# Optimization experiments

Measured on AMD Instinct MI355X. Metric: run time of the kernel, lower is better.

The kernel has to match this reference:

```python
import jax, jax.numpy as jnp
import numpy as np

B = 131072
UNITS = 256
INPUT_DIM = 256


def setup_inputs() -> dict:
    key = jax.random.key(0)
    ks = jax.random.split(key, 8)
    x = jax.random.normal(ks[0], (B, INPUT_DIM), dtype=jnp.float32)
    h_prev = jax.random.normal(ks[1], (B, UNITS), dtype=jnp.float32)
    c_prev = jax.random.normal(ks[2], (B, UNITS), dtype=jnp.float32)
    # glorot-like scale for W: fan_in = INPUT_DIM + UNITS, fan_out = 4*UNITS
    scale = jnp.sqrt(2.0 / (INPUT_DIM + UNITS + 4 * UNITS)).astype(jnp.float32)
    W = jax.random.normal(ks[3], (INPUT_DIM + UNITS, 4 * UNITS), dtype=jnp.float32) * scale
    # bias: zeros except forget gate initialized to 1.0
    b = jnp.concatenate([
        jnp.zeros(UNITS, jnp.float32),
        jnp.ones(UNITS, jnp.float32),
        jnp.zeros(UNITS, jnp.float32),
        jnp.zeros(UNITS, jnp.float32),
    ])
    peephole_i = jax.random.normal(ks[4], (UNITS,), dtype=jnp.float32) * 0.05
    peephole_f = jax.random.normal(ks[5], (UNITS,), dtype=jnp.float32) * 0.05
    peephole_o = jax.random.normal(ks[6], (UNITS,), dtype=jnp.float32) * 0.05
    return {
        "x": x, "h_prev": h_prev, "c_prev": c_prev,
        "W": W, "b": b,
        "peephole_i": peephole_i, "peephole_f": peephole_f, "peephole_o": peephole_o,
    }


def reference(x, h_prev, c_prev, W, b, peephole_i, peephole_f, peephole_o):
    combined = jnp.concatenate([x, h_prev], axis=-1)          # [B, INPUT_DIM+UNITS]
    z = combined @ W + b                                      # [B, 4*UNITS]
    i, f, c_hat, o = jnp.split(z, 4, axis=1)                  # each [B, UNITS]
    i = jax.nn.sigmoid(i + peephole_i * c_prev)
    f = jax.nn.sigmoid(f + peephole_f * c_prev)
    o = jax.nn.sigmoid(o + peephole_o * c_prev)
    c_hat = jnp.tanh(c_hat)
    c = f * c_prev + i * c_hat
    h = o * jnp.tanh(c)
    return (h, h, c)  # matches (output, [h, c]) of the Keras cell
```

## Files before the change

kernel.cpp:

```cpp
#include <hip/hip_runtime.h>
#include <cstdint>

#define NROWS   131072
#define NUNITS  256
#define KTOT    512
#define BM      128
#define THREADS 512

typedef float f32x4  __attribute__((ext_vector_type(4)));
typedef short bf16x8 __attribute__((ext_vector_type(8)));

__device__ __forceinline__ short f2bf(float x) {
    unsigned u = __float_as_uint(x);
    u += 0x7FFFu + ((u >> 16) & 1u);
    return (short)(u >> 16);
}

__global__ void convert_kernel(const float* __restrict__ x, const float* __restrict__ h,
                               const float* __restrict__ W,
                               short* __restrict__ Aws, short* __restrict__ Wws) {
    int b = blockIdx.x;
    if (b < 32768) {
        int i = b * 256 + threadIdx.x;
        int row = i >> 6;
        int c   = (i & 63) * 4;
        float4 xv = *(const float4*)(x + (size_t)row * 256 + c);
        float4 hv = *(const float4*)(h + (size_t)row * 256 + c);
        short xs[4] = {f2bf(xv.x), f2bf(xv.y), f2bf(xv.z), f2bf(xv.w)};
        short hs[4] = {f2bf(hv.x), f2bf(hv.y), f2bf(hv.z), f2bf(hv.w)};
        *(uint2*)(Aws + (size_t)row * 512 + c)       = *(uint2*)xs;
        *(uint2*)(Aws + (size_t)row * 512 + 256 + c) = *(uint2*)hs;
    } else {
        int i = (b - 32768) * 256 + threadIdx.x;
        int k = i >> 10;
        int c = i & 1023;
        Wws[((size_t)(k >> 5) << 15) + ((size_t)c << 5) + (k & 31)] = f2bf(W[i]);
    }
}

__global__ void __launch_bounds__(THREADS, 4)
lstm_main_kernel(const float* __restrict__ c_prev, const float* __restrict__ bias,
                 const float* __restrict__ pi, const float* __restrict__ pf,
                 const float* __restrict__ po, const short* __restrict__ Aws,
                 const short* __restrict__ Wws, float* __restrict__ out) {
    __shared__ short lds[3][12288];

    const int bid = blockIdx.x;
    const int swz = (bid & 7) * 512 + (bid >> 3);
    const int ut  = swz & 3;
    const int rt  = swz >> 2;
    const int row0 = rt * BM;

    const int t    = threadIdx.x;
    const int lane = t & 63;
    const int w    = t >> 6;
    const int lr   = lane & 15;
    const int hi   = lane >> 4;
    const int rh   = w >> 2;
    const int q    = w & 3;

    const int arow = t >> 2, ags = t & 3;
    const short* srcA = Aws + (size_t)(row0 + arow) * 512 + ((ags ^ (arow & 3)) * 8);
    const int G1 = t + 512;
    const int g0 = t >> 8,  u0 = (t >> 2) & 63,  s0 = t & 3;
    const int g1 = G1 >> 8, u1 = (G1 >> 2) & 63, s1 = G1 & 3;
    const short* srcB0 = Wws + (size_t)(g0 * 256 + ut * 64 + u0) * 32 + ((s0 ^ (u0 & 3)) * 8);
    const short* srcB1 = Wws + (size_t)(g1 * 256 + ut * 64 + u1) * 32 + ((s1 ^ (u1 & 3)) * 8);

    const int sw8  = (hi ^ (lr & 3)) * 8;
    const int aoff = (rh * 64 + lr) * 32 + sw8;
    const int boff = 4096 + (q * 16 + lr) * 32 + sw8;

    f32x4 acc[4][4];
    #pragma unroll
    for (int m = 0; m < 4; ++m)
        #pragma unroll
        for (int g = 0; g < 4; ++g)
            acc[m][g] = (f32x4){0.f, 0.f, 0.f, 0.f};

    auto issueDMA = [&](int ks, int buf) {
        short* dst = &lds[buf][0];
        __builtin_amdgcn_global_load_lds(
            (const __attribute__((address_space(1))) uint32_t*)(const void*)(srcA + ks * 32),
            (__attribute__((address_space(3))) uint32_t*)(void*)(dst + w * 512), 16, 0, 0);
        __builtin_amdgcn_global_load_lds(
            (const __attribute__((address_space(1))) uint32_t*)(const void*)(srcB0 + (size_t)ks * 32768),
            (__attribute__((address_space(3))) uint32_t*)(void*)(dst + 4096 + w * 512), 16, 0, 0);
        __builtin_amdgcn_global_load_lds(
            (const __attribute__((address_space(1))) uint32_t*)(const void*)(srcB1 + (size_t)ks * 32768),
            (__attribute__((address_space(3))) uint32_t*)(void*)(dst + 8192 + w * 512), 16, 0, 0);
    };

    auto compute = [&](int buf) {
        const short* L = &lds[buf][0];
        bf16x8 af[4], bfr[4];
        #pragma unroll
        for (int m = 0; m < 4; ++m)
            af[m] = *(const bf16x8*)&L[aoff + m * 512];
        #pragma unroll
        for (int g = 0; g < 4; ++g)
            bfr[g] = *(const bf16x8*)&L[boff + g * 2048];
        #pragma unroll
        for (int g = 0; g < 4; ++g)
            #pragma unroll
            for (int m = 0; m < 4; ++m)
                acc[m][g] = __builtin_amdgcn_mfma_f32_16x16x32_bf16(af[m], bfr[g], acc[m][g], 0, 0, 0);
    };

    issueDMA(0, 0);
    issueDMA(1, 1);

    int cur = 0;
    #pragma unroll 1
    for (int p = 0; p < 16; ++p) {
        if (p < 15) { asm volatile("s_waitcnt vmcnt(3)" ::: "memory"); }
        else        { asm volatile("s_waitcnt vmcnt(0)" ::: "memory"); }
        __builtin_amdgcn_s_barrier();
        if (p < 14) {
            int nb = cur + 2; if (nb >= 3) nb -= 3;
            issueDMA(p + 2, nb);
        }
        compute(cur);
        if (++cur == 3) cur = 0;
    }

    const size_t HS = (size_t)NROWS * NUNITS;
    const int u = ut * 64 + q * 16 + lr;
    const float bi = bias[u],       bfg = bias[256 + u];
    const float bc = bias[512 + u], bo  = bias[768 + u];
    const float ppi = pi[u], ppf = pf[u], ppo = po[u];
    #pragma unroll
    for (int m = 0; m < 4; ++m) {
        #pragma unroll
        for (int r = 0; r < 4; ++r) {
            const int row = row0 + rh * 64 + m * 16 + hi * 4 + r;
            const size_t o = (size_t)row * NUNITS + u;
            const float cp = c_prev[o];
            float zi = acc[m][0][r] + bi  + ppi * cp;
            float zf = acc[m][1][r] + bfg + ppf * cp;
            float zc = acc[m][2][r] + bc;
            float zo = acc[m][3][r] + bo  + ppo * cp;
            float ig = 1.f / (1.f + __expf(-zi));
            float fg = 1.f / (1.f + __expf(-zf));
            float og = 1.f / (1.f + __expf(-zo));
            zc = fminf(fmaxf(zc, -30.f), 30.f);
            float e2 = __expf(2.f * zc);
            float chat = (e2 - 1.f) / (e2 + 1.f);
            float c  = fg * cp + ig * chat;
            float ccl = fminf(fmaxf(c, -30.f), 30.f);
            float e3 = __expf(2.f * ccl);
            float th = (e3 - 1.f) / (e3 + 1.f);
            float h  = og * th;
            out[o]          = h;
            out[HS + o]     = h;
            out[2 * HS + o] = c;
        }
    }
}

extern "C" void kernel_launch(void* const* d_in, const int* in_sizes, int n_in,
                              void* d_out, int out_size, void* d_ws, size_t ws_size,
                              hipStream_t stream) {
    const float* x  = (const float*)d_in[0];
    const float* h  = (const float*)d_in[1];
    const float* c  = (const float*)d_in[2];
    const float* W  = (const float*)d_in[3];
    const float* b  = (const float*)d_in[4];
    const float* pi = (const float*)d_in[5];
    const float* pf = (const float*)d_in[6];
    const float* po = (const float*)d_in[7];
    float* out = (float*)d_out;

    const size_t aws_bytes = (size_t)NROWS * KTOT * 2;
    short* Aws = (short*)d_ws;
    short* Wws = (short*)((char*)d_ws + aws_bytes);

    hipLaunchKernelGGL(convert_kernel, dim3(32768 + 2048), dim3(256), 0, stream,
                       x, h, W, Aws, Wws);
    hipLaunchKernelGGL(lstm_main_kernel, dim3(NROWS / BM * 4), dim3(THREADS), 0, stream,
                       c, b, pi, pf, po, Aws, Wws, out);
}
```

Measured before the change: 322.1 us.

## Double M tile to 256 rows with K=64 double-buffered LDS stages

The row tile grows from 128 to 256 per block, so each wave computes 8x4 MFMA tiles and every B fragment is reused across more A rows. The K step per stage goes from 32 to 64, and the LDS pipeline changes from a triple buffer with a distance of two to a double buffer with a full vmcnt(0) wait each iteration. The LDS swizzle pattern changes and s_setprio is placed around the MFMA bursts. The goal is to cut W reloads and barrier count per FLOP, at the cost of more registers, lower occupancy (launch bounds 2), and less latency hiding from the shallower prefetch.

```diff
diff --git a/kernel.cpp b/kernel.cpp
--- a/kernel.cpp
+++ b/kernel.cpp
@@ -4,7 +4,7 @@
 #define NROWS   131072
 #define NUNITS  256
 #define KTOT    512
-#define BM      128
+#define BM      256
 #define THREADS 512
 
 typedef float f32x4  __attribute__((ext_vector_type(4)));
@@ -38,15 +38,15 @@
     }
 }
 
-__global__ void __launch_bounds__(THREADS, 4)
+__global__ void __launch_bounds__(THREADS, 2)
 lstm_main_kernel(const float* __restrict__ c_prev, const float* __restrict__ bias,
                  const float* __restrict__ pi, const float* __restrict__ pf,
                  const float* __restrict__ po, const short* __restrict__ Aws,
                  const short* __restrict__ Wws, float* __restrict__ out) {
-    __shared__ short lds[3][12288];
+    __shared__ short lds[2][32768];
 
     const int bid = blockIdx.x;
-    const int swz = (bid & 7) * 512 + (bid >> 3);
+    const int swz = (bid & 7) * 256 + (bid >> 3);
     const int ut  = swz & 3;
     const int rt  = swz >> 2;
     const int row0 = rt * BM;
@@ -59,69 +59,77 @@
     const int rh   = w >> 2;
     const int q    = w & 3;
 
-    const int arow = t >> 2, ags = t & 3;
-    const short* srcA = Aws + (size_t)(row0 + arow) * 512 + ((ags ^ (arow & 3)) * 8);
-    const int G1 = t + 512;
-    const int g0 = t >> 8,  u0 = (t >> 2) & 63,  s0 = t & 3;
-    const int g1 = G1 >> 8, u1 = (G1 >> 2) & 63, s1 = G1 & 3;
-    const short* srcB0 = Wws + (size_t)(g0 * 256 + ut * 64 + u0) * 32 + ((s0 ^ (u0 & 3)) * 8);
-    const short* srcB1 = Wws + (size_t)(g1 * 256 + ut * 64 + u1) * 32 + ((s1 ^ (u1 & 3)) * 8);
+    const short* srcA[2];
+    const short* srcB[2];
+    #pragma unroll
+    for (int rep = 0; rep < 2; ++rep) {
+        const int G    = rep * 512 + t;
+        const int arow = G >> 2, ag = G & 3;
+        srcA[rep] = Aws + (size_t)(row0 + arow) * 512 + ((ag ^ ((arow >> 1) & 3)) * 8);
+        const int cp = G >> 2, bg = G & 3;
+        const int gate = cp >> 6, u64 = cp & 63;
+        srcB[rep] = Wws + (size_t)(gate * 256 + ut * 64 + u64) * 32
+                        + ((bg ^ ((cp >> 1) & 3)) * 8);
+    }
 
-    const int sw8  = (hi ^ (lr & 3)) * 8;
-    const int aoff = (rh * 64 + lr) * 32 + sw8;
-    const int boff = 4096 + (q * 16 + lr) * 32 + sw8;
+    const int sw    = (hi ^ ((lr >> 1) & 3)) * 8;
+    const int abase = (rh * 128 + lr) * 32 + sw;
+    const int bbase = 16384 + (q * 16 + lr) * 32 + sw;
 
-    f32x4 acc[4][4];
+    f32x4 acc[8][4];
     #pragma unroll
-    for (int m = 0; m < 4; ++m)
+    for (int m = 0; m < 8; ++m)
         #pragma unroll
         for (int g = 0; g < 4; ++g)
             acc[m][g] = (f32x4){0.f, 0.f, 0.f, 0.f};
 
-    auto issueDMA = [&](int ks, int buf) {
-        short* dst = &lds[buf][0];
-        __builtin_amdgcn_global_load_lds(
-            (const __attribute__((address_space(1))) uint32_t*)(const void*)(srcA + ks * 32),
-            (__attribute__((address_space(3))) uint32_t*)(void*)(dst + w * 512), 16, 0, 0);
-        __builtin_amdgcn_global_load_lds(
-            (const __attribute__((address_space(1))) uint32_t*)(const void*)(srcB0 + (size_t)ks * 32768),
-            (__attribute__((address_space(3))) uint32_t*)(void*)(dst + 4096 + w * 512), 16, 0, 0);
-        __builtin_amdgcn_global_load_lds(
-            (const __attribute__((address_space(1))) uint32_t*)(const void*)(srcB1 + (size_t)ks * 32768),
-            (__attribute__((address_space(3))) uint32_t*)(void*)(dst + 8192 + w * 512), 16, 0, 0);
+    auto dma = [&](int kt, int buf) {
+        short* base = &lds[buf][0];
+        #pragma unroll
+        for (int rep = 0; rep < 2; ++rep)
+            #pragma unroll
+            for (int kk = 0; kk < 2; ++kk) {
+                __builtin_amdgcn_global_load_lds(
+                    (const __attribute__((address_space(1))) uint32_t*)(const void*)
+                        (srcA[rep] + kt * 64 + kk * 32),
+                    (__attribute__((address_space(3))) uint32_t*)(void*)
+                        (base + kk * 8192 + (rep * 512 + t) * 8), 16, 0, 0);
+                __builtin_amdgcn_global_load_lds(
+                    (const __attribute__((address_space(1))) uint32_t*)(const void*)
+                        (srcB[rep] + (size_t)(kt * 2 + kk) * 32768),
+                    (__attribute__((address_space(3))) uint32_t*)(void*)
+                        (base + 16384 + kk * 8192 + (rep * 512 + t) * 8), 16, 0, 0);
+            }
     };
 
     auto compute = [&](int buf) {
         const short* L = &lds[buf][0];
-        bf16x8 af[4], bfr[4];
         #pragma unroll
-        for (int m = 0; m < 4; ++m)
-            af[m] = *(const bf16x8*)&L[aoff + m * 512];
-        #pragma unroll
-        for (int g = 0; g < 4; ++g)
-            bfr[g] = *(const bf16x8*)&L[boff + g * 2048];
-        #pragma unroll
-        for (int g = 0; g < 4; ++g)
+        for (int kk = 0; kk < 2; ++kk) {
+            bf16x8 bfr[4], af[8];
             #pragma unroll
-            for (int m = 0; m < 4; ++m)
-                acc[m][g] = __builtin_amdgcn_mfma_f32_16x16x32_bf16(af[m], bfr[g], acc[m][g], 0, 0, 0);
+            for (int g = 0; g < 4; ++g)
+                bfr[g] = *(const bf16x8*)&L[bbase + kk * 8192 + g * 2048];
+            #pragma unroll
+            for (int m = 0; m < 8; ++m)
+                af[m] = *(const bf16x8*)&L[abase + kk * 8192 + m * 512];
+            __builtin_amdgcn_s_setprio(1);
+            #pragma unroll
+            for (int g = 0; g < 4; ++g)
+                #pragma unroll
+                for (int m = 0; m < 8; ++m)
+                    acc[m][g] = __builtin_amdgcn_mfma_f32_16x16x32_bf16(af[m], bfr[g], acc[m][g], 0, 0, 0);
+            __builtin_amdgcn_s_setprio(0);
+        }
     };
 
-    issueDMA(0, 0);
-    issueDMA(1, 1);
-
-    int cur = 0;
+    dma(0, 0);
     #pragma unroll 1
-    for (int p = 0; p < 16; ++p) {
-        if (p < 15) { asm volatile("s_waitcnt vmcnt(3)" ::: "memory"); }
-        else        { asm volatile("s_waitcnt vmcnt(0)" ::: "memory"); }
+    for (int kt = 0; kt < 8; ++kt) {
+        asm volatile("s_waitcnt vmcnt(0)" ::: "memory");
         __builtin_amdgcn_s_barrier();
-        if (p < 14) {
-            int nb = cur + 2; if (nb >= 3) nb -= 3;
-            issueDMA(p + 2, nb);
-        }
-        compute(cur);
-        if (++cur == 3) cur = 0;
+        if (kt < 7) dma(kt + 1, (kt + 1) & 1);
+        compute(kt & 1);
     }
 
     const size_t HS = (size_t)NROWS * NUNITS;
@@ -130,10 +138,10 @@
     const float bc = bias[512 + u], bo  = bias[768 + u];
     const float ppi = pi[u], ppf = pf[u], ppo = po[u];
     #pragma unroll
-    for (int m = 0; m < 4; ++m) {
+    for (int m = 0; m < 8; ++m) {
         #pragma unroll
         for (int r = 0; r < 4; ++r) {
-            const int row = row0 + rh * 64 + m * 16 + hi * 4 + r;
+            const int row = row0 + rh * 128 + m * 16 + hi * 4 + r;
             const size_t o = (size_t)row * NUNITS + u;
             const float cp = c_prev[o];
             float zi = acc[m][0][r] + bi  + ppi * cp;
```

Measured after the change: 350.8 us. 1.09x slower.

## Fuse activation bf16 conversion into GEMM main loop, loading fp32 A directly

Applied to the files above, without the earlier changes.

Drops the separate pass that converted x and h_prev to a bf16 workspace. The main kernel now streams fp32 activation tiles into LDS (triple-buffered, XOR-swizzled) and converts them to bf16 in registers with v_cvt_pk_bf16_f32 before the MFMAs, while weights are double-buffered separately. This removes a full write and re-read of a 128 MB bf16 copy, but each block, and each of the four unit-tile blocks sharing a row tile, now reads fp32 A at twice the byte width and does extra conversion work per k-step. It also raises MFMA issue priority with s_setprio around the MFMA loop.

```diff
diff --git a/kernel.cpp b/kernel.cpp
--- a/kernel.cpp
+++ b/kernel.cpp
@@ -16,34 +16,21 @@
     return (short)(u >> 16);
 }
 
-__global__ void convert_kernel(const float* __restrict__ x, const float* __restrict__ h,
-                               const float* __restrict__ W,
-                               short* __restrict__ Aws, short* __restrict__ Wws) {
-    int b = blockIdx.x;
-    if (b < 32768) {
-        int i = b * 256 + threadIdx.x;
-        int row = i >> 6;
-        int c   = (i & 63) * 4;
-        float4 xv = *(const float4*)(x + (size_t)row * 256 + c);
-        float4 hv = *(const float4*)(h + (size_t)row * 256 + c);
-        short xs[4] = {f2bf(xv.x), f2bf(xv.y), f2bf(xv.z), f2bf(xv.w)};
-        short hs[4] = {f2bf(hv.x), f2bf(hv.y), f2bf(hv.z), f2bf(hv.w)};
-        *(uint2*)(Aws + (size_t)row * 512 + c)       = *(uint2*)xs;
-        *(uint2*)(Aws + (size_t)row * 512 + 256 + c) = *(uint2*)hs;
-    } else {
-        int i = (b - 32768) * 256 + threadIdx.x;
-        int k = i >> 10;
-        int c = i & 1023;
-        Wws[((size_t)(k >> 5) << 15) + ((size_t)c << 5) + (k & 31)] = f2bf(W[i]);
-    }
+__global__ void convert_W_kernel(const float* __restrict__ W, short* __restrict__ Wws) {
+    int i = blockIdx.x * 256 + threadIdx.x;
+    int k = i >> 10;
+    int c = i & 1023;
+    Wws[((size_t)(k >> 5) << 15) + ((size_t)c << 5) + (k & 31)] = f2bf(W[i]);
 }
 
 __global__ void __launch_bounds__(THREADS, 4)
-lstm_main_kernel(const float* __restrict__ c_prev, const float* __restrict__ bias,
+lstm_main_kernel(const float* __restrict__ x, const float* __restrict__ h_prev,
+                 const float* __restrict__ c_prev, const float* __restrict__ bias,
                  const float* __restrict__ pi, const float* __restrict__ pf,
-                 const float* __restrict__ po, const short* __restrict__ Aws,
-                 const short* __restrict__ Wws, float* __restrict__ out) {
-    __shared__ short lds[3][12288];
+                 const float* __restrict__ po, const short* __restrict__ Wws,
+                 float* __restrict__ out) {
+    __shared__ float Alds[3][4096];
+    __shared__ short Blds[2][8192];
 
     const int bid = blockIdx.x;
     const int swz = (bid & 7) * 512 + (bid >> 3);
@@ -59,17 +46,27 @@
     const int rh   = w >> 2;
     const int q    = w & 3;
 
-    const int arow = t >> 2, ags = t & 3;
-    const short* srcA = Aws + (size_t)(row0 + arow) * 512 + ((ags ^ (arow & 3)) * 8);
-    const int G1 = t + 512;
-    const int g0 = t >> 8,  u0 = (t >> 2) & 63,  s0 = t & 3;
-    const int g1 = G1 >> 8, u1 = (G1 >> 2) & 63, s1 = G1 & 3;
-    const short* srcB0 = Wws + (size_t)(g0 * 256 + ut * 64 + u0) * 32 + ((s0 ^ (u0 & 3)) * 8);
-    const short* srcB1 = Wws + (size_t)(g1 * 256 + ut * 64 + u1) * 32 + ((s1 ^ (u1 & 3)) * 8);
+    const float* aX[2]; const float* aH[2];
+    #pragma unroll
+    for (int rep = 0; rep < 2; ++rep) {
+        const int G = rep * 512 + t;
+        const int r = G >> 3, s = G & 7, g = s ^ (r & 7);
+        aX[rep] = x      + (size_t)(row0 + r) * 256 + g * 4;
+        aH[rep] = h_prev + (size_t)(row0 + r) * 256 + g * 4;
+    }
+    const short* srcB[2];
+    #pragma unroll
+    for (int rep = 0; rep < 2; ++rep) {
+        const int G = rep * 512 + t;
+        const int cp = G >> 2, bg = G & 3;
+        const int gate = cp >> 6, u64 = cp & 63;
+        srcB[rep] = Wws + (size_t)(gate * 256 + ut * 64 + u64) * 32
+                        + ((bg ^ ((cp >> 1) & 3)) * 8);
+    }
 
-    const int sw8  = (hi ^ (lr & 3)) * 8;
-    const int aoff = (rh * 64 + lr) * 32 + sw8;
-    const int boff = 4096 + (q * 16 + lr) * 32 + sw8;
+    const int s0    = (2 * hi) ^ (lr & 7);
+    const int bsw   = (hi ^ ((lr >> 1) & 3)) * 8;
+    const int boff  = (q * 16 + lr) * 32 + bsw;
 
     f32x4 acc[4][4];
     #pragma unroll
@@ -78,50 +75,71 @@
         for (int g = 0; g < 4; ++g)
             acc[m][g] = (f32x4){0.f, 0.f, 0.f, 0.f};
 
-    auto issueDMA = [&](int ks, int buf) {
-        short* dst = &lds[buf][0];
+    auto dmaA = [&](int ks, int buf) {
+        const int off = (ks & 7) * 32;
+        const float* p0 = (ks < 8 ? aX[0] : aH[0]) + off;
+        const float* p1 = (ks < 8 ? aX[1] : aH[1]) + off;
+        float* dst = &Alds[buf][0];
         __builtin_amdgcn_global_load_lds(
-            (const __attribute__((address_space(1))) uint32_t*)(const void*)(srcA + ks * 32),
-            (__attribute__((address_space(3))) uint32_t*)(void*)(dst + w * 512), 16, 0, 0);
+            (const __attribute__((address_space(1))) uint32_t*)(const void*)p0,
+            (__attribute__((address_space(3))) uint32_t*)(void*)(dst + t * 4), 16, 0, 0);
         __builtin_amdgcn_global_load_lds(
-            (const __attribute__((address_space(1))) uint32_t*)(const void*)(srcB0 + (size_t)ks * 32768),
-            (__attribute__((address_space(3))) uint32_t*)(void*)(dst + 4096 + w * 512), 16, 0, 0);
+            (const __attribute__((address_space(1))) uint32_t*)(const void*)p1,
+            (__attribute__((address_space(3))) uint32_t*)(void*)(dst + 2048 + t * 4), 16, 0, 0);
+    };
+    auto dmaB = [&](int ks, int buf) {
+        short* dst = &Blds[buf][0];
         __builtin_amdgcn_global_load_lds(
-            (const __attribute__((address_space(1))) uint32_t*)(const void*)(srcB1 + (size_t)ks * 32768),
-            (__attribute__((address_space(3))) uint32_t*)(void*)(dst + 8192 + w * 512), 16, 0, 0);
+            (const __attribute__((address_space(1))) uint32_t*)(const void*)(srcB[0] + (size_t)ks * 32768),
+            (__attribute__((address_space(3))) uint32_t*)(void*)(dst + t * 8), 16, 0, 0);
+        __builtin_amdgcn_global_load_lds(
+            (const __attribute__((address_space(1))) uint32_t*)(const void*)(srcB[1] + (size_t)ks * 32768),
+            (__attribute__((address_space(3))) uint32_t*)(void*)(dst + 4096 + t * 8), 16, 0, 0);
     };
 
-    auto compute = [&](int buf) {
-        const short* L = &lds[buf][0];
+    auto compute = [&](int abuf, int bbuf) {
+        const float* A = &Alds[abuf][0];
+        const short* B = &Blds[bbuf][0];
         bf16x8 af[4], bfr[4];
         #pragma unroll
-        for (int m = 0; m < 4; ++m)
-            af[m] = *(const bf16x8*)&L[aoff + m * 512];
+        for (int m = 0; m < 4; ++m) {
+            const int r = rh * 64 + m * 16 + lr;
+            f32x4 lo = *(const f32x4*)&A[r * 32 + s0 * 4];
+            f32x4 hi4 = *(const f32x4*)&A[r * 32 + (s0 ^ 1) * 4];
+            unsigned u0, u1, u2, u3;
+            asm("v_cvt_pk_bf16_f32 %0, %1, %2" : "=v"(u0) : "v"(lo[0]),  "v"(lo[1]));
+            asm("v_cvt_pk_bf16_f32 %0, %1, %2" : "=v"(u1) : "v"(lo[2]),  "v"(lo[3]));
+            asm("v_cvt_pk_bf16_f32 %0, %1, %2" : "=v"(u2) : "v"(hi4[0]), "v"(hi4[1]));
+            asm("v_cvt_pk_bf16_f32 %0, %1, %2" : "=v"(u3) : "v"(hi4[2]), "v"(hi4[3]));
+            unsigned uu[4] = {u0, u1, u2, u3};
+            af[m] = *(bf16x8*)uu;
+        }
         #pragma unroll
         for (int g = 0; g < 4; ++g)
-            bfr[g] = *(const bf16x8*)&L[boff + g * 2048];
+            bfr[g] = *(const bf16x8*)&B[boff + g * 2048];
+        __builtin_amdgcn_s_setprio(1);
         #pragma unroll
         for (int g = 0; g < 4; ++g)
             #pragma unroll
             for (int m = 0; m < 4; ++m)
                 acc[m][g] = __builtin_amdgcn_mfma_f32_16x16x32_bf16(af[m], bfr[g], acc[m][g], 0, 0, 0);
+        __builtin_amdgcn_s_setprio(0);
     };
 
-    issueDMA(0, 0);
-    issueDMA(1, 1);
+    dmaA(0, 0);
+    dmaB(0, 0);
+    dmaA(1, 1);
 
-    int cur = 0;
+    int ab = 0;
     #pragma unroll 1
     for (int p = 0; p < 16; ++p) {
-        if (p < 15) { asm volatile("s_waitcnt vmcnt(3)" ::: "memory"); }
+        if (p < 15) { asm volatile("s_waitcnt vmcnt(2)" ::: "memory"); }
         else        { asm volatile("s_waitcnt vmcnt(0)" ::: "memory"); }
         __builtin_amdgcn_s_barrier();
-        if (p < 14) {
-            int nb = cur + 2; if (nb >= 3) nb -= 3;
-            issueDMA(p + 2, nb);
-        }
-        compute(cur);
-        if (++cur == 3) cur = 0;
+        if (p < 15) dmaB(p + 1, (p + 1) & 1);
+        if (p < 14) { int nb = ab + 2; if (nb >= 3) nb -= 3; dmaA(p + 2, nb); }
+        compute(ab, p & 1);
+        if (++ab == 3) ab = 0;
     }
 
     const size_t HS = (size_t)NROWS * NUNITS;
@@ -171,12 +189,9 @@
     const float* po = (const float*)d_in[7];
     float* out = (float*)d_out;
 
-    const size_t aws_bytes = (size_t)NROWS * KTOT * 2;
-    short* Aws = (short*)d_ws;
-    short* Wws = (short*)((char*)d_ws + aws_bytes);
+    short* Wws = (short*)d_ws;
 
-    hipLaunchKernelGGL(convert_kernel, dim3(32768 + 2048), dim3(256), 0, stream,
-                       x, h, W, Aws, Wws);
+    hipLaunchKernelGGL(convert_W_kernel, dim3(2048), dim3(256), 0, stream, W, Wws);
     hipLaunchKernelGGL(lstm_main_kernel, dim3(NROWS / BM * 4), dim3(THREADS), 0, stream,
-                       c, b, pi, pf, po, Aws, Wws, out);
+                       x, h, c, b, pi, pf, po, Wws, out);
 }
```

New measurement: 322.2 us. Within noise of the previous version (+0.1%).
